# Performance work log

Measured on AMD Instinct MI355X. Metric: run time of the kernel, lower is better.

The kernel has to match this reference:

```python
import jax, jax.numpy as jnp
import numpy as np

B, T, C, H = 2, 2048, 1024, 16
D = C // H
EPS = 1e-5

def _layer_norm(x, w, b):
    mu = jnp.mean(x, axis=-1, keepdims=True)
    var = jnp.var(x, axis=-1, keepdims=True)
    return (x - mu) * jax.lax.rsqrt(var + EPS) * w + b

def setup_inputs() -> dict:
    key = jax.random.key(0)
    ks = jax.random.split(key, 8)
    s = 0.02
    return {
        "x": jax.random.normal(ks[0], (B, T, C), jnp.float32),
        "ln1_w": jnp.ones((C,), jnp.float32),
        "ln1_b": jnp.zeros((C,), jnp.float32),
        "wq": jax.random.normal(ks[1], (C, C), jnp.float32) * s,
        "bq": jnp.zeros((C,), jnp.float32),
        "wk": jax.random.normal(ks[2], (C, C), jnp.float32) * s,
        "bk": jnp.zeros((C,), jnp.float32),
        "wv": jax.random.normal(ks[3], (C, C), jnp.float32) * s,
        "bv": jnp.zeros((C,), jnp.float32),
        "wo": jax.random.normal(ks[4], (C, C), jnp.float32) * s,
        "bo": jnp.zeros((C,), jnp.float32),
        "ln2_w": jnp.ones((C,), jnp.float32),
        "ln2_b": jnp.zeros((C,), jnp.float32),
        "w1": jax.random.normal(ks[5], (C, 4 * C), jnp.float32) * s,
        "b1": jnp.zeros((4 * C,), jnp.float32),
        "w2": jax.random.normal(ks[6], (4 * C, C), jnp.float32) * s,
        "b2": jnp.zeros((C,), jnp.float32),
    }

def reference(x, ln1_w, ln1_b, wq, bq, wk, bk, wv, bv, wo, bo,
              ln2_w, ln2_b, w1, b1, w2, b2):
    # --- attention branch ---
    h = _layer_norm(x, ln1_w, ln1_b)
    q = (h @ wq + bq).reshape(B, T, H, D).transpose(0, 2, 1, 3)  # [B,H,T,D]
    k = (h @ wk + bk).reshape(B, T, H, D).transpose(0, 2, 1, 3)
    v = (h @ wv + bv).reshape(B, T, H, D).transpose(0, 2, 1, 3)
    att = jnp.einsum("bhqd,bhkd->bhqk", q, k) * (1.0 / np.sqrt(D))
    causal = jnp.tril(jnp.ones((T, T), dtype=bool))
    att = jnp.where(causal[None, None], att, jnp.float32(-jnp.inf))
    att = jax.nn.softmax(att, axis=-1)
    y = jnp.einsum("bhqk,bhkd->bhqd", att, v)
    y = y.transpose(0, 2, 1, 3).reshape(B, T, C)
    y = y @ wo + bo
    x = x + y
    # --- MLP branch ---
    h = _layer_norm(x, ln2_w, ln2_b)
    h = jax.nn.gelu(h @ w1 + b1, approximate=False)
    h = h @ w2 + b2
    return x + h
```

## Files before the change

kernel.cpp:

```cpp
#include <hip/hip_runtime.h>
#include <hip/hip_bf16.h>
#include <math.h>

#define B_  2
#define T_  2048
#define C_  1024
#define H_  16
#define D_  64
#define BT_ (B_*T_)

typedef __hip_bfloat16 bf16;
typedef short bf16x8 __attribute__((ext_vector_type(8)));
typedef float floatx4 __attribute__((ext_vector_type(4)));

struct alignas(8) bf4 { bf16 v[4]; };

#define GLOAD_LDS16(g, l) __builtin_amdgcn_global_load_lds(            \
    (const __attribute__((address_space(1))) void*)(g),                \
    (__attribute__((address_space(3))) void*)(l), 16, 0, 0)

__global__ __launch_bounds__(256) void ln_bf16_kernel(const float* __restrict__ x,
    const float* __restrict__ w, const float* __restrict__ b,
    bf16* __restrict__ out)
{
    __shared__ float ps[4], ps2[4];
    __shared__ float sm, srs;
    const int row = blockIdx.x;
    const int tid = threadIdx.x;
    float4 v = ((const float4*)(x + (size_t)row * C_))[tid];
    float s  = v.x + v.y + v.z + v.w;
    float s2 = v.x*v.x + v.y*v.y + v.z*v.z + v.w*v.w;
    for (int off = 32; off > 0; off >>= 1) {
        s  += __shfl_down(s,  off);
        s2 += __shfl_down(s2, off);
    }
    const int wid = tid >> 6;
    if ((tid & 63) == 0) { ps[wid] = s; ps2[wid] = s2; }
    __syncthreads();
    if (tid == 0) {
        float ts  = ps[0] + ps[1] + ps[2] + ps[3];
        float ts2 = ps2[0] + ps2[1] + ps2[2] + ps2[3];
        float mean = ts * (1.0f / C_);
        float var  = ts2 * (1.0f / C_) - mean * mean;
        sm  = mean;
        srs = rsqrtf(var + 1e-5f);
    }
    __syncthreads();
    const float mean = sm, rs = srs;
    float4 wv = ((const float4*)w)[tid];
    float4 bv = ((const float4*)b)[tid];
    bf4 o;
    o.v[0] = __float2bfloat16((v.x - mean) * rs * wv.x + bv.x);
    o.v[1] = __float2bfloat16((v.y - mean) * rs * wv.y + bv.y);
    o.v[2] = __float2bfloat16((v.z - mean) * rs * wv.z + bv.z);
    o.v[3] = __float2bfloat16((v.w - mean) * rs * wv.w + bv.w);
    *(bf4*)(out + (size_t)row * C_ + tid * 4) = o;
}

__device__ __forceinline__ void wconv_body(const float* __restrict__ W,
    bf16* __restrict__ Wt, int K, int N, int k0, int n0)
{
    __shared__ float L[64][65];
    const int t = threadIdx.x;
    const int r = t >> 4, c4 = t & 15;
    #pragma unroll
    for (int p = 0; p < 4; ++p) {
        const int kr = p * 16 + r;
        const float4 v = *(const float4*)(W + (size_t)(k0 + kr) * N + n0 + c4 * 4);
        L[kr][c4*4+0] = v.x; L[kr][c4*4+1] = v.y;
        L[kr][c4*4+2] = v.z; L[kr][c4*4+3] = v.w;
    }
    __syncthreads();
    #pragma unroll
    for (int p = 0; p < 4; ++p) {
        const int nr = p * 16 + r;
        bf4 o;
        o.v[0] = __float2bfloat16(L[c4*4+0][nr]);
        o.v[1] = __float2bfloat16(L[c4*4+1][nr]);
        o.v[2] = __float2bfloat16(L[c4*4+2][nr]);
        o.v[3] = __float2bfloat16(L[c4*4+3][nr]);
        *(bf4*)(Wt + (size_t)(n0 + nr) * K + k0 + c4 * 4) = o;
    }
}

__global__ __launch_bounds__(256) void wconv4_kernel(
    const float* __restrict__ wq, const float* __restrict__ wk,
    const float* __restrict__ wv, const float* __restrict__ wo,
    bf16* __restrict__ wqkvT, bf16* __restrict__ woT)
{
    const int z = blockIdx.z;
    const float* W = (z == 0) ? wq : (z == 1) ? wk : (z == 2) ? wv : wo;
    bf16* Wt = (z == 3) ? woT : wqkvT + (size_t)z * 1024 * 1024;
    wconv_body(W, Wt, 1024, 1024, blockIdx.x * 64, blockIdx.y * 64);
}

__global__ __launch_bounds__(256) void wconv2_kernel(
    const float* __restrict__ w1, const float* __restrict__ w2,
    bf16* __restrict__ w1T, bf16* __restrict__ w2T)
{
    if (blockIdx.z == 0)
        wconv_body(w1, w1T, 1024, 4096, blockIdx.x * 64, blockIdx.y * 64);
    else
        wconv_body(w2, w2T, 4096, 1024, blockIdx.y * 64, blockIdx.x * 64);
}

__global__ void bcat_kernel(const float* __restrict__ bq, const float* __restrict__ bk,
                            const float* __restrict__ bv, float* __restrict__ o)
{
    const int i = blockIdx.x * 256 + threadIdx.x;
    float v = (i < 1024) ? bq[i] : (i < 2048 ? bk[i - 1024] : bv[i - 2048]);
    o[i] = v;
}

__global__ __launch_bounds__(256) void splitk_reduce_kernel(
    float* __restrict__ out, const float* __restrict__ p1,
    const float* __restrict__ bias, const float* __restrict__ res)
{
    const size_t i = (size_t)blockIdx.x * 256 + threadIdx.x;
    float4 o = ((const float4*)out)[i];
    const float4 p = ((const float4*)p1)[i];
    const float4 bb = ((const float4*)bias)[i & (C_ / 4 - 1)];
    const float4 xx = ((const float4*)res)[i];
    o.x += p.x + bb.x + xx.x;
    o.y += p.y + bb.y + xx.y;
    o.z += p.z + bb.z + xx.z;
    o.w += p.w + bb.w + xx.w;
    ((float4*)out)[i] = o;
}

template<int TM, int TN, int BK>
__global__ __launch_bounds__(256) void mfma_gemm_t(
    const bf16* __restrict__ A, const bf16* __restrict__ Wt,
    const float* __restrict__ bias, const float* __restrict__ res,
    void* __restrict__ outv, bf16* __restrict__ vT, float* __restrict__ psplit,
    int M, int N, int K, int ldk, int mode)
{
    constexpr int MI = TM / 32;
    constexpr int NJ = TN / 32;
    constexpr int CPR = BK / 8;
    constexpr int NSLOT = (TM + TN) * CPR / 256;
    __shared__ __align__(16) bf16 smem[(TM + TN) * BK];
    bf16* As = smem;
    bf16* Bs = smem + TM * BK;
    const int tid = threadIdx.x;
    const int w = tid >> 6, l = tid & 63;
    const int fm = l & 15, qd = l >> 4;
    const int m0 = blockIdx.x * TM, n0 = blockIdx.y * TN;
    const int bz = blockIdx.z;
    const int wr = (w >> 1) * (TM / 2), wc = (w & 1) * (TN / 2);

    const bf16* Ab = A  + (size_t)bz * K;
    const bf16* Wb = Wt + (size_t)bz * K;

    const bf16* gsrc[NSLOT];
    bf16* ldst[NSLOT];
    #pragma unroll
    for (int p = 0; p < NSLOT; ++p) {
        const int s = tid + p * 256;
        if (s < TM * CPR) {
            const int row = s / CPR, pos = s % CPR;
            const int ch = pos ^ (row & (CPR - 1));
            gsrc[p] = Ab + (size_t)(m0 + row) * ldk + ch * 8;
            ldst[p] = As + s * 8;
        } else {
            const int s2 = s - TM * CPR;
            const int row = s2 / CPR, pos = s2 % CPR;
            const int ch = pos ^ (row & (CPR - 1));
            gsrc[p] = Wb + (size_t)(n0 + row) * ldk + ch * 8;
            ldst[p] = Bs + s2 * 8;
        }
    }

    floatx4 acc[MI][NJ] = {};

    const int nk = K / BK;
    for (int kk = 0; kk < nk; ++kk) {
        const size_t ko = (size_t)kk * BK;
        __syncthreads();
        #pragma unroll
        for (int p = 0; p < NSLOT; ++p)
            GLOAD_LDS16(gsrc[p] + ko, ldst[p]);
        __syncthreads();
        #pragma unroll
        for (int ks = 0; ks < BK / 32; ++ks) {
            bf16x8 af[MI], bfr[NJ];
            #pragma unroll
            for (int i = 0; i < MI; ++i) {
                const int row = wr + i * 16 + fm;
                af[i] = *(const bf16x8*)(As + row * BK
                        + (((ks * 4 + qd) ^ (row & (CPR - 1))) * 8));
            }
            #pragma unroll
            for (int j = 0; j < NJ; ++j) {
                const int row = wc + j * 16 + fm;
                bfr[j] = *(const bf16x8*)(Bs + row * BK
                        + (((ks * 4 + qd) ^ (row & (CPR - 1))) * 8));
            }
            #pragma unroll
            for (int i = 0; i < MI; ++i)
                #pragma unroll
                for (int j = 0; j < NJ; ++j)
                    acc[i][j] = __builtin_amdgcn_mfma_f32_16x16x32_bf16(
                        af[i], bfr[j], acc[i][j], 0, 0, 0);
        }
    }

    const int col0 = n0 + wc;
    const int row0 = m0 + wr;
    const bool isv = (mode == 3) && (col0 >= 2048);
    const bool bounce = (mode == 0) || (mode == 1) || (mode == 3 && !isv);
    __syncthreads();

    if (bounce) {
        constexpr int RM = TM / 2, RN = TN / 2, CHN = RN / 8;
        bf16* eb = smem + w * (RM * RN);
        #pragma unroll
        for (int j = 0; j < NJ; ++j) {
            const int col = col0 + j * 16 + fm;
            const float bb = bias[col];
            const bool isq = (mode == 3) && (col0 + j * 16 < 1024);
            const int lc = j * 16 + fm;
            #pragma unroll
            for (int i = 0; i < MI; ++i) {
                floatx4 a = acc[i][j];
                #pragma unroll
                for (int r = 0; r < 4; ++r) {
                    float vv = a[r] + bb;
                    if (mode == 1) {
                        float zz = vv * (0.7978845608f + 0.0356774081f * vv * vv);
                        zz = fminf(zz, 15.0f);
                        const float e = __expf(2.0f * zz);
                        vv = vv * (e / (e + 1.0f));
                    }
                    if (isq) vv *= 0.125f;
                    const int lr = i * 16 + qd * 4 + r;
                    const int pch = ((lc >> 3) + 2 * qd) & (CHN - 1);
                    eb[lr * RN + pch * 8 + (lc & 7)] = __float2bfloat16(vv);
                }
            }
        }
        bf16* o = (bf16*)outv;
        #pragma unroll
        for (int c = 0; c < RM * RN / 512; ++c) {
            const int idx = c * 64 + l;
            const int row = idx / CHN;
            const int c8  = idx % CHN;
            const int pch = (c8 + 2 * ((row >> 2) & 3)) & (CHN - 1);
            const bf16x8 vv = *(const bf16x8*)(eb + row * RN + pch * 8);
            *(bf16x8*)(o + (size_t)(row0 + row) * N + col0 + c8 * 8) = vv;
        }
    } else {
        #pragma unroll
        for (int j = 0; j < NJ; ++j) {
            const int col = col0 + j * 16 + fm;
            const float bb = bias[col];
            #pragma unroll
            for (int i = 0; i < MI; ++i) {
                const int row = row0 + i * 16 + qd * 4;
                floatx4 a = acc[i][j];
                if (mode == 4) {
                    float* o = bz ? psplit : (float*)outv;
                    #pragma unroll
                    for (int r = 0; r < 4; ++r)
                        o[(size_t)(row + r) * N + col] = a[r];
                } else if (mode == 2) {
                    float* o = (float*)outv;
                    #pragma unroll
                    for (int r = 0; r < 4; ++r)
                        o[(size_t)(row + r) * N + col] =
                            a[r] + bb + res[(size_t)(row + r) * N + col];
                } else {
                    bf4 pv;
                    #pragma unroll
                    for (int r = 0; r < 4; ++r) pv.v[r] = __float2bfloat16(a[r] + bb);
                    *(bf4*)(vT + (size_t)(col - 2048) * M + row) = pv;
                }
            }
        }
    }
}


#define G8_BARRIER() do {                                   \
    __builtin_amdgcn_sched_barrier(0);                      \
    asm volatile("" ::: "memory");                          \
    __builtin_amdgcn_s_barrier();                           \
    asm volatile("" ::: "memory");                          \
    __builtin_amdgcn_sched_barrier(0);                      \
  } while (0)

#define G8_WAIT_LGKM0() do {                                        \
    asm volatile("s_waitcnt lgkmcnt(0)" ::: "memory");              \
    __builtin_amdgcn_sched_barrier(0);                              \
  } while (0)

#define G8_WAIT_VM(n) asm volatile("s_waitcnt vmcnt(" #n ")" ::: "memory")

#define G8_PHASE(Aq, Bq, G, VW)                                                \
  do {                                                                         \
    const bf16* pa0 = smem + cur * BUF + aof0 + (Aq) * 8192;                   \
    const bf16* pa1 = smem + cur * BUF + aof1 + (Aq) * 8192;                   \
    const bf16* pb0 = smem + cur * BUF + bof0 + (Bq) * 2048;                   \
    const bf16* pb1 = smem + cur * BUF + bof1 + (Bq) * 2048;                   \
    bf16x8 af[4][2], bv[2][2];                                                 \
    _Pragma("unroll")                                                          \
    for (int i = 0; i < 4; ++i) {                                              \
      af[i][0] = *(const bf16x8*)(pa0 + i * 1024);                             \
      af[i][1] = *(const bf16x8*)(pa1 + i * 1024);                             \
    }                                                                          \
    _Pragma("unroll")                                                          \
    for (int jj = 0; jj < 2; ++jj) {                                           \
      bv[jj][0] = *(const bf16x8*)(pb0 + jj * 1024);                           \
      bv[jj][1] = *(const bf16x8*)(pb1 + jj * 1024);                           \
    }                                                                          \
    if (st) {                                                                  \
      GLOAD_LDS16(gsrc[(G)*2]     + ko, smem + nb * BUF + lof[(G)*2]);         \
      GLOAD_LDS16(gsrc[(G)*2 + 1] + ko, smem + nb * BUF + lof[(G)*2 + 1]);     \
    }                                                                          \
    G8_BARRIER();                                                              \
    G8_WAIT_LGKM0();                                                           \
    __builtin_amdgcn_s_setprio(1);                                             \
    _Pragma("unroll")                                                          \
    for (int i = 0; i < 4; ++i)                                                \
      _Pragma("unroll")                                                        \
      for (int jj = 0; jj < 2; ++jj) {                                         \
        acc[(Aq)*4+i][(Bq)*2+jj] = __builtin_amdgcn_mfma_f32_16x16x32_bf16(    \
            af[i][0], bv[jj][0], acc[(Aq)*4+i][(Bq)*2+jj], 0, 0, 0);           \
        acc[(Aq)*4+i][(Bq)*2+jj] = __builtin_amdgcn_mfma_f32_16x16x32_bf16(    \
            af[i][1], bv[jj][1], acc[(Aq)*4+i][(Bq)*2+jj], 0, 0, 0);           \
      }                                                                        \
    __builtin_amdgcn_s_setprio(0);                                             \
    VW;                                                                        \
    G8_BARRIER();                                                              \
  } while (0)

template<int MODE>
__global__ __launch_bounds__(512, 2) void gemm8_t(
    const bf16* __restrict__ A, const bf16* __restrict__ Wt,
    const float* __restrict__ bias, bf16* __restrict__ out,
    bf16* __restrict__ vT, int M, int N, int K)
{
    constexpr int BUF = 32768;
    __shared__ __align__(16) bf16 smem[2 * BUF];

    const int tid = threadIdx.x;
    const int w = tid >> 6, l = tid & 63;
    const int fm = l & 15, qd = l >> 4;
    const int wm = w >> 2, wn = w & 3;

    const int nbx = gridDim.x;
    const int nwg = nbx * gridDim.y;
    const int bid = blockIdx.y * nbx + blockIdx.x;
    const int cpx = nwg >> 3;
    const int swz = (bid & 7) * cpx + (bid >> 3);
    const int m0 = (swz % nbx) * 256;
    const int n0 = (swz / nbx) * 256;

    const bf16* gsrc[8];
    int lof[8];
    #pragma unroll
    for (int g = 0; g < 4; ++g) {
        const bf16* gb = (g < 2) ? (Wt + (size_t)(n0 + (g & 1) * 128) * K)
                                 : (A  + (size_t)(m0 + (g & 1) * 128) * K);
        const int lbase = (g < 2) ? (16384 + (g & 1) * 8192) : ((g & 1) * 8192);
        #pragma unroll
        for (int s = 0; s < 2; ++s) {
            const int c = tid + s * 512;
            const int row = c >> 3, pos = c & 7;
            const int ch = pos ^ (row & 7);
            gsrc[g * 2 + s] = gb + (size_t)row * K + ch * 8;
            lof[g * 2 + s] = lbase + c * 8;
        }
    }

    const int sw0 = qd ^ (fm & 7);
    const int aof0 = (wm * 64 + fm) * 64 + sw0 * 8;
    const int aof1 = (wm * 64 + fm) * 64 + (sw0 ^ 4) * 8;
    const int bof0 = 16384 + (wn * 64 + fm) * 64 + sw0 * 8;
    const int bof1 = 16384 + (wn * 64 + fm) * 64 + (sw0 ^ 4) * 8;

    floatx4 acc[8][4] = {};

    #pragma unroll
    for (int s = 0; s < 8; ++s)
        GLOAD_LDS16(gsrc[s], smem + lof[s]);
    G8_WAIT_VM(2);
    G8_BARRIER();

    const int nt = K / 64;
    int cur = 0;
    for (int t = 0; t < nt; ++t, cur ^= 1) {
        const bool st = (t + 1 < nt);
        const int nb = cur ^ 1;
        const size_t ko = (size_t)(t + 1) * 64;
        G8_PHASE(0, 0, 0, ;);
        G8_PHASE(0, 1, 1, do { if (st) { G8_WAIT_VM(4); } else { G8_WAIT_VM(0); } } while (0));
        G8_PHASE(1, 0, 2, ;);
        G8_PHASE(1, 1, 3, G8_WAIT_VM(2));
    }

    G8_WAIT_VM(0);
    G8_BARRIER();

    const int colb = n0 + wn * 64;
    if (MODE == 3 && colb >= 2048) {
        #pragma unroll
        for (int jf = 0; jf < 4; ++jf) {
            const int col = colb + jf * 16 + fm;
            const float bb = bias[col];
            #pragma unroll
            for (int f = 0; f < 8; ++f) {
                const int row = m0 + (f >> 2) * 128 + wm * 64 + (f & 3) * 16 + qd * 4;
                bf4 pv;
                #pragma unroll
                for (int r = 0; r < 4; ++r)
                    pv.v[r] = __float2bfloat16(acc[f][jf][r] + bb);
                *(bf4*)(vT + (size_t)(col - 2048) * M + row) = pv;
            }
        }
    } else {
        const float scale = (MODE == 3 && colb < 1024) ? 0.125f : 1.0f;
        bf16* eb = smem + w * 8192;
        #pragma unroll
        for (int jf = 0; jf < 4; ++jf) {
            const int col = colb + jf * 16 + fm;
            const float bb = bias[col];
            const int lc = jf * 16 + fm;
            const int pch = ((lc >> 3) + 2 * qd) & 7;
            #pragma unroll
            for (int f = 0; f < 8; ++f) {
                const int lr = (f & 3) * 16 + qd * 4;
                #pragma unroll
                for (int r = 0; r < 4; ++r) {
                    float vv = acc[f][jf][r] + bb;
                    if (MODE == 1) {
                        float zz = vv * (0.7978845608f + 0.0356774081f * vv * vv);
                        zz = fminf(zz, 15.0f);
                        const float e = __expf(2.0f * zz);
                        vv = vv * (e / (e + 1.0f));
                    }
                    vv *= scale;
                    eb[(f >> 2) * 4096 + (lr + r) * 64 + pch * 8 + (lc & 7)] =
                        __float2bfloat16(vv);
                }
            }
        }
        #pragma unroll
        for (int p = 0; p < 2; ++p)
            #pragma unroll
            for (int c = 0; c < 8; ++c) {
                const int idx = c * 64 + l;
                const int row = idx >> 3, c8 = idx & 7;
                const int pch = (c8 + 2 * ((row >> 2) & 3)) & 7;
                const bf16x8 vv = *(const bf16x8*)(eb + p * 4096 + row * 64 + pch * 8);
                const int rowg = m0 + p * 128 + wm * 64 + row;
                *(bf16x8*)(out + (size_t)rowg * N + colb + c8 * 8) = vv;
            }
    }
}

__global__ __launch_bounds__(256) void attn_mfma_kernel(
    const bf16* __restrict__ qkv, const bf16* __restrict__ vT,
    bf16* __restrict__ y)
{
    const int pi = blockIdx.x, h = blockIdx.y, b = blockIdx.z;
    const int tid = threadIdx.x, w = tid >> 6, l = tid & 63;
    const int fm = l & 15, qd = l >> 4;
    const int qta = pi, qtb = 31 - pi;
    const float M0 = 3.0f;

    __shared__ __align__(16) bf16 Ks[4096];
    __shared__ __align__(16) bf16 Vs[4096];
    __shared__ __align__(16) bf16 Ps[8][1152];

    const int r0 = tid >> 2,         c0 = (tid & 3) ^ ((r0 >> 1) & 3);
    const int r1 = (tid + 256) >> 2, c1 = ((tid + 256) & 3) ^ ((r1 >> 1) & 3);
    const bf16* kbase = qkv + (size_t)(b * T_) * 3072 + 1024 + h * 64;
    const bf16* vbase = vT + (size_t)(h * 64) * BT_ + b * T_;
    const bf16* kg0 = kbase + (size_t)(r0 & 63) * 3072 + (r0 >> 6) * 32 + c0 * 8;
    const bf16* kg1 = kbase + (size_t)(r1 & 63) * 3072 + (r1 >> 6) * 32 + c1 * 8;
    const bf16* vg0 = vbase + (size_t)(r0 & 63) * BT_ + (r0 >> 6) * 32 + c0 * 8;
    const bf16* vg1 = vbase + (size_t)(r1 & 63) * BT_ + (r1 >> 6) * 32 + c1 * 8;
    bf16* ksl0 = Ks + (size_t)(w * 64) * 8;
    bf16* ksl1 = Ks + (size_t)(w * 64 + 256) * 8;
    bf16* vsl0 = Vs + (size_t)(w * 64) * 8;
    bf16* vsl1 = Vs + (size_t)(w * 64 + 256) * 8;

    const bf16* qpa = qkv + (size_t)(b * T_ + qta * 64 + w * 16 + fm) * 3072 + h * 64 + qd * 8;
    const bf16* qpb = qkv + (size_t)(b * T_ + qtb * 64 + w * 16 + fm) * 3072 + h * 64 + qd * 8;
    const bf16x8 qa0 = *(const bf16x8*)qpa, qa1 = *(const bf16x8*)(qpa + 32);
    const bf16x8 qb0 = *(const bf16x8*)qpb, qb1 = *(const bf16x8*)(qpb + 32);

    const int qba = qta * 64 + w * 16 + qd * 4;
    const int qbb = qtb * 64 + w * 16 + qd * 4;
    const int sw = (qd ^ ((fm >> 1) & 3)) * 8;

    float la[4] = {}, lb[4] = {};
    floatx4 Oa[4] = {}, Ob[4] = {};
    bf16* psa = &Ps[w * 2][0];
    bf16* psb = &Ps[w * 2 + 1][0];

    auto tile = [&](const bf16x8 q0, const bf16x8 q1, float* lsum,
                    floatx4* O, bf16* ps, const int kt, const int qt, const int qb) {
        floatx4 S[4];
        #pragma unroll
        for (int nt = 0; nt < 4; ++nt) {
            const int rr = nt * 16 + fm;
            const bf16x8 k0 = *(const bf16x8*)(Ks + rr * 32 + sw);
            const bf16x8 k1 = *(const bf16x8*)(Ks + (64 + rr) * 32 + sw);
            floatx4 s = {};
            s = __builtin_amdgcn_mfma_f32_16x16x32_bf16(q0, k0, s, 0, 0, 0);
            s = __builtin_amdgcn_mfma_f32_16x16x32_bf16(q1, k1, s, 0, 0, 0);
            S[nt] = s;
        }
        if (kt == qt) {
            #pragma unroll
            for (int nt = 0; nt < 4; ++nt) {
                const int key = kt * 64 + nt * 16 + fm;
                #pragma unroll
                for (int r = 0; r < 4; ++r)
                    if (key > qb + r) S[nt][r] = -1e30f;
            }
        }
        #pragma unroll
        for (int nt = 0; nt < 4; ++nt)
            #pragma unroll
            for (int r = 0; r < 4; ++r) {
                const float p = __expf(S[nt][r] - M0);
                lsum[r] += p;
                ps[(qd * 4 + r) * 72 + nt * 16 + fm] = __float2bfloat16(p);
            }
        #pragma unroll
        for (int s2 = 0; s2 < 2; ++s2) {
            const bf16x8 pf = *(const bf16x8*)(ps + fm * 72 + s2 * 32 + qd * 8);
            #pragma unroll
            for (int nt = 0; nt < 4; ++nt) {
                const bf16x8 vf =
                    *(const bf16x8*)(Vs + (s2 * 64 + nt * 16 + fm) * 32 + sw);
                O[nt] = __builtin_amdgcn_mfma_f32_16x16x32_bf16(pf, vf, O[nt], 0, 0, 0);
            }
        }
    };

    for (int kt = 0; kt <= qtb; ++kt) {
        const size_t kOff = (size_t)kt * 64 * 3072;
        const size_t vOff = (size_t)kt * 64;
        __syncthreads();
        GLOAD_LDS16(kg0 + kOff, ksl0);
        GLOAD_LDS16(kg1 + kOff, ksl1);
        GLOAD_LDS16(vg0 + vOff, vsl0);
        GLOAD_LDS16(vg1 + vOff, vsl1);
        __syncthreads();
        tile(qb0, qb1, lb, Ob, psb, kt, qtb, qbb);
        if (kt <= qta)
            tile(qa0, qa1, la, Oa, psa, kt, qta, qba);
    }

    #pragma unroll
    for (int mk = 1; mk < 16; mk <<= 1)
        #pragma unroll
        for (int r = 0; r < 4; ++r) {
            la[r] += __shfl_xor(la[r], mk);
            lb[r] += __shfl_xor(lb[r], mk);
        }

    #pragma unroll
    for (int r = 0; r < 4; ++r) {
        const float inva = 1.0f / la[r];
        const float invb = 1.0f / lb[r];
        const size_t rowa = (size_t)(b * T_) + qba + r;
        const size_t rowb = (size_t)(b * T_) + qbb + r;
        #pragma unroll
        for (int nt = 0; nt < 4; ++nt) {
            y[rowa * C_ + h * 64 + nt * 16 + fm] = __float2bfloat16(Oa[nt][r] * inva);
            y[rowb * C_ + h * 64 + nt * 16 + fm] = __float2bfloat16(Ob[nt][r] * invb);
        }
    }
}

extern "C" void kernel_launch(void* const* d_in, const int* in_sizes, int n_in,
                              void* d_out, int out_size, void* d_ws, size_t ws_size,
                              hipStream_t stream)
{
    const float* x     = (const float*)d_in[0];
    const float* ln1_w = (const float*)d_in[1];
    const float* ln1_b = (const float*)d_in[2];
    const float* wq    = (const float*)d_in[3];
    const float* bq    = (const float*)d_in[4];
    const float* wk    = (const float*)d_in[5];
    const float* bk    = (const float*)d_in[6];
    const float* wv    = (const float*)d_in[7];
    const float* bv    = (const float*)d_in[8];
    const float* wo    = (const float*)d_in[9];
    const float* bo    = (const float*)d_in[10];
    const float* ln2_w = (const float*)d_in[11];
    const float* ln2_b = (const float*)d_in[12];
    const float* w1    = (const float*)d_in[13];
    const float* b1    = (const float*)d_in[14];
    const float* w2    = (const float*)d_in[15];
    const float* b2    = (const float*)d_in[16];
    float* out = (float*)d_out;

    char* ws = (char*)d_ws;
    const size_t MB = 1024 * 1024;
    bf16*  wqkvT = (bf16*)(ws);
    bf16*  woT   = (bf16*)(ws + 6 * MB);
    bf16*  w1T   = (bf16*)(ws + 8 * MB);
    bf16*  w2T   = (bf16*)(ws + 16 * MB);
    float* bqkv  = (float*)(ws + 24 * MB);
    bf16*  h     = (bf16*)(ws + 24 * MB + 65536);
    bf16*  qkv   = (bf16*)(ws + 32 * MB + 65536);
    bf16*  vT    = (bf16*)(ws + 56 * MB + 65536);
    bf16*  y     = (bf16*)(ws + 64 * MB + 65536);
    float* x2    = (float*)(ws + 72 * MB + 65536);
    bf16*  u     = qkv;
    float* p1    = (float*)ws;

    wconv4_kernel<<<dim3(16, 16, 4), 256, 0, stream>>>(wq, wk, wv, wo, wqkvT, woT);
    wconv2_kernel<<<dim3(16, 64, 2), 256, 0, stream>>>(w1, w2, w1T, w2T);
    bcat_kernel<<<12, 256, 0, stream>>>(bq, bk, bv, bqkv);

    ln_bf16_kernel<<<BT_, 256, 0, stream>>>(x, ln1_w, ln1_b, h);
    gemm8_t<3><<<dim3(16, 12), 512, 0, stream>>>(
        h, wqkvT, bqkv, qkv, vT, BT_, 3072, C_);
    attn_mfma_kernel<<<dim3(16, H_, B_), 256, 0, stream>>>(qkv, vT, y);
    mfma_gemm_t<128, 64, 64><<<dim3(32, 16), 256, 0, stream>>>(
        y, woT, bo, x, x2, nullptr, nullptr, BT_, C_, C_, C_, 2);

    ln_bf16_kernel<<<BT_, 256, 0, stream>>>(x2, ln2_w, ln2_b, h);
    gemm8_t<1><<<dim3(16, 16), 512, 0, stream>>>(
        h, w1T, b1, u, nullptr, BT_, 4 * C_, C_);
    mfma_gemm_t<128, 128, 64><<<dim3(32, 8, 2), 256, 0, stream>>>(
        u, w2T, b2, nullptr, out, nullptr, p1, BT_, C_, 2 * C_, 4 * C_, 4);
    splitk_reduce_kernel<<<BT_ * C_ / 1024, 256, 0, stream>>>(out, p1, b2, x2);
}
```

Measured before the change: 364.8 us.

## Deepen GEMM prefetch by staging B-tile halves two k-steps ahead

Rearranges the LDS load mapping so each load group covers one half of the A or B tile, then reorders the four MFMA phases so B-halves that are no longer read in the current buffer are refilled with data for k-step t+2. Wait counts are retuned so more global loads are in flight across the barriers. This is meant to hide more global-to-LDS latency. In exchange the vmcnt bookkeeping gets more fragile, and a wrong count could race on the shared buffer.

Measured after the change: 355.9 us. 2.4% less time.

```diff
diff --git a/kernel.cpp b/kernel.cpp
--- a/kernel.cpp
+++ b/kernel.cpp
@@ -296,7 +296,12 @@
 
 #define G8_WAIT_VM(n) asm volatile("s_waitcnt vmcnt(" #n ")" ::: "memory")
 
-#define G8_PHASE(Aq, Bq, G, VW)                                                \
+#define G8_VW2() do { if (st1) G8_WAIT_VM(8); else G8_WAIT_VM(2); } while (0)
+#define G8_VW3() do { if (st1) G8_WAIT_VM(8); else G8_WAIT_VM(0); } while (0)
+#define G8_VW1() do { if (st2) G8_WAIT_VM(8); else if (st1) G8_WAIT_VM(4); \
+                      else G8_WAIT_VM(0); } while (0)
+
+#define G8_PHASE(Aq, Bq, SC, SG, DB, KO, VW)                                   \
   do {                                                                         \
     const bf16* pa0 = smem + cur * BUF + aof0 + (Aq) * 8192;                   \
     const bf16* pa1 = smem + cur * BUF + aof1 + (Aq) * 8192;                   \
@@ -313,9 +318,9 @@
       bv[jj][0] = *(const bf16x8*)(pb0 + jj * 1024);                           \
       bv[jj][1] = *(const bf16x8*)(pb1 + jj * 1024);                           \
     }                                                                          \
-    if (st) {                                                                  \
-      GLOAD_LDS16(gsrc[(G)*2]     + ko, smem + nb * BUF + lof[(G)*2]);         \
-      GLOAD_LDS16(gsrc[(G)*2 + 1] + ko, smem + nb * BUF + lof[(G)*2 + 1]);     \
+    if (SC) {                                                                  \
+      GLOAD_LDS16(gsrc[(SG)*2]     + (KO), smem + (DB) * BUF + lof[(SG)*2]);   \
+      GLOAD_LDS16(gsrc[(SG)*2 + 1] + (KO), smem + (DB) * BUF + lof[(SG)*2+1]); \
     }                                                                          \
     G8_BARRIER();                                                              \
     G8_WAIT_LGKM0();                                                           \
@@ -360,16 +365,27 @@
     int lof[8];
     #pragma unroll
     for (int g = 0; g < 4; ++g) {
-        const bf16* gb = (g < 2) ? (Wt + (size_t)(n0 + (g & 1) * 128) * K)
-                                 : (A  + (size_t)(m0 + (g & 1) * 128) * K);
-        const int lbase = (g < 2) ? (16384 + (g & 1) * 8192) : ((g & 1) * 8192);
+        const int isB  = (g & 1);
+        const int half = (g >> 1);
         #pragma unroll
         for (int s = 0; s < 2; ++s) {
             const int c = tid + s * 512;
-            const int row = c >> 3, pos = c & 7;
+            const int pos = c & 7;
+            int row, lofe;
+            const bf16* gb;
+            if (!isB) {
+                row  = half * 128 + (c >> 3);
+                gb   = A + (size_t)(m0 + row) * K;
+                lofe = row * 64 + pos * 8;
+            } else {
+                const int vr = c >> 3;
+                row  = (vr >> 5) * 64 + half * 32 + (vr & 31);
+                gb   = Wt + (size_t)(n0 + row) * K;
+                lofe = 16384 + row * 64 + pos * 8;
+            }
             const int ch = pos ^ (row & 7);
-            gsrc[g * 2 + s] = gb + (size_t)row * K + ch * 8;
-            lof[g * 2 + s] = lbase + c * 8;
+            gsrc[g * 2 + s] = gb + ch * 8;
+            lof[g * 2 + s]  = lofe;
         }
     }
 
@@ -382,21 +398,27 @@
     floatx4 acc[8][4] = {};
 
     #pragma unroll
-    for (int s = 0; s < 8; ++s)
-        GLOAD_LDS16(gsrc[s], smem + lof[s]);
-    G8_WAIT_VM(2);
+    for (int s2 = 0; s2 < 8; ++s2)
+        GLOAD_LDS16(gsrc[s2], smem + lof[s2]);
+    GLOAD_LDS16(gsrc[2] + 64, smem + BUF + lof[2]);
+    GLOAD_LDS16(gsrc[3] + 64, smem + BUF + lof[3]);
+    GLOAD_LDS16(gsrc[0] + 64, smem + BUF + lof[0]);
+    GLOAD_LDS16(gsrc[1] + 64, smem + BUF + lof[1]);
+    G8_WAIT_VM(8);
     G8_BARRIER();
 
     const int nt = K / 64;
     int cur = 0;
     for (int t = 0; t < nt; ++t, cur ^= 1) {
-        const bool st = (t + 1 < nt);
+        const bool st1 = (t + 1 < nt);
+        const bool st2 = (t + 2 < nt);
         const int nb = cur ^ 1;
-        const size_t ko = (size_t)(t + 1) * 64;
-        G8_PHASE(0, 0, 0, ;);
-        G8_PHASE(0, 1, 1, do { if (st) { G8_WAIT_VM(4); } else { G8_WAIT_VM(0); } } while (0));
-        G8_PHASE(1, 0, 2, ;);
-        G8_PHASE(1, 1, 3, G8_WAIT_VM(2));
+        const size_t ko1 = (size_t)(t + 1) * 64;
+        const size_t ko2 = (size_t)(t + 2) * 64;
+        G8_PHASE(0, 0, st1, 2, nb,  ko1, G8_VW2());
+        G8_PHASE(1, 0, st1, 3, nb,  ko1, G8_VW3());
+        G8_PHASE(0, 1, st2, 1, cur, ko2, ;);
+        G8_PHASE(1, 1, st2, 0, cur, ko2, G8_VW1());
     }
 
     G8_WAIT_VM(0);
```
